# Performance work log

Hardware: AMD Instinct MI355X
Metric: run time of the kernel (lower is better)

Reference implementation:

```python
import jax, jax.numpy as jnp
import numpy as np

B, N = 65536, 128

def setup_inputs() -> dict:
    key = jax.random.key(0)
    k1, k2, k3, k4, k5 = jax.random.split(key, 5)
    density = jax.random.uniform(k1, (B, N), dtype=jnp.float32) * 10.0   # nonneg densities
    deltas = jax.random.uniform(k2, (B, N), dtype=jnp.float32) * 0.05 + 1e-3  # positive step sizes
    zs = jnp.cumsum(deltas, axis=-1) + 2.0                               # monotone sample depths
    raw_rgbs = jax.random.uniform(k4, (B, N, 3), dtype=jnp.float32)
    raw_normals = jax.random.normal(k5, (B, N, 3), dtype=jnp.float32)
    return {"density": density, "deltas": deltas, "zs": zs,
            "raw_rgbs": raw_rgbs, "raw_normals": raw_normals}


def reference(density, deltas, zs, raw_rgbs, raw_normals):
    # alpha -> transmittance (exclusive cumprod) -> weight
    alpha = 1.0 - jnp.exp(-density * deltas)                 # [B, N]
    one_minus = 1.0 - alpha
    cp = jnp.cumprod(one_minus, axis=-1)                     # inclusive cumprod
    trans = jnp.concatenate([jnp.ones_like(cp[:, :1]), cp[:, :-1]], axis=-1)  # exclusive
    weight = alpha * trans                                   # [B, N]

    # composites
    rgb = jnp.einsum('bn,bnc->bc', weight, raw_rgbs)         # [B, 3]
    acc = jnp.sum(weight, axis=1, keepdims=True)             # [B, 1]
    depth = jnp.sum(weight * zs, axis=1, keepdims=True) / (acc + 1e-8)  # normalized
    normal = jnp.einsum('bn,bnc->bc', weight, raw_normals)   # [B, 3]

    # pack outputs: rgb(3) | depth(1) | normal(3) | acc(1) -> [B, 8]
    return jnp.concatenate([rgb, depth, normal, acc], axis=-1)
```

## Files before the change

### kernel.cpp

```cpp
#include <hip/hip_runtime.h>


constexpr int RAYS = 65536;
constexpr int NS   = 128;

__global__ __launch_bounds__(256) void render_composite_kernel(
    const float* __restrict__ density,
    const float* __restrict__ deltas,
    const float* __restrict__ zs,
    const float* __restrict__ rgbs,
    const float* __restrict__ normals,
    float* __restrict__ out)
{
    const int lane = threadIdx.x & 63;
    const int wave = threadIdx.x >> 6;
    const int ray  = blockIdx.x * 4 + wave;
    if (ray >= RAYS) return;

    const size_t row  = (size_t)ray * NS;
    const size_t row3 = (size_t)ray * NS * 3;

    const float2 d  = reinterpret_cast<const float2*>(density + row)[lane];
    const float2 dl = reinterpret_cast<const float2*>(deltas  + row)[lane];
    const float2 z  = reinterpret_cast<const float2*>(zs      + row)[lane];

    const float s0 = d.x * dl.x;
    const float s1 = d.y * dl.y;
    const float slocal = s0 + s1;

    float prefix = slocal;
    #pragma unroll
    for (int off = 1; off < 64; off <<= 1) {
        float up = __shfl_up(prefix, off, 64);
        if (lane >= off) prefix += up;
    }
    const float S_base = prefix - slocal;

    const float e0 = __expf(-S_base);
    const float e1 = __expf(-(S_base + s0));
    const float e2 = __expf(-(S_base + s0 + s1));
    const float w0 = e0 - e1;
    const float w1 = e1 - e2;

    const float2* rg2 = reinterpret_cast<const float2*>(rgbs    + row3) + lane * 3;
    const float2* nm2 = reinterpret_cast<const float2*>(normals + row3) + lane * 3;
    const float2 ra = rg2[0], rb = rg2[1], rc = rg2[2];
    const float2 na = nm2[0], nb = nm2[1], nc = nm2[2];

    float acc_r = w0 * ra.x + w1 * rb.y;
    float acc_g = w0 * ra.y + w1 * rc.x;
    float acc_b = w0 * rb.x + w1 * rc.y;
    float acc_nr = w0 * na.x + w1 * nb.y;
    float acc_ng = w0 * na.y + w1 * nc.x;
    float acc_nb = w0 * nb.x + w1 * nc.y;
    float acc_w  = w0 + w1;
    float acc_wz = w0 * z.x + w1 * z.y;

    #pragma unroll
    for (int off = 32; off > 0; off >>= 1) {
        acc_r  += __shfl_xor(acc_r,  off, 64);
        acc_g  += __shfl_xor(acc_g,  off, 64);
        acc_b  += __shfl_xor(acc_b,  off, 64);
        acc_nr += __shfl_xor(acc_nr, off, 64);
        acc_ng += __shfl_xor(acc_ng, off, 64);
        acc_nb += __shfl_xor(acc_nb, off, 64);
        acc_w  += __shfl_xor(acc_w,  off, 64);
        acc_wz += __shfl_xor(acc_wz, off, 64);
    }

    if (lane == 0) {
        const float depth = acc_wz / (acc_w + 1e-8f);
        float4* o = reinterpret_cast<float4*>(out + (size_t)ray * 8);
        o[0] = make_float4(acc_r, acc_g, acc_b, depth);
        o[1] = make_float4(acc_nr, acc_ng, acc_nb, acc_w);
    }
}

extern "C" void kernel_launch(void* const* d_in, const int* in_sizes, int n_in,
                              void* d_out, int out_size, void* d_ws, size_t ws_size,
                              hipStream_t stream) {
    const float* density = (const float*)d_in[0];
    const float* deltas  = (const float*)d_in[1];
    const float* zs      = (const float*)d_in[2];
    const float* rgbs    = (const float*)d_in[3];
    const float* normals = (const float*)d_in[4];
    float* out = (float*)d_out;

    const int waves_per_block = 4;
    const int grid = RAYS / waves_per_block;
    render_composite_kernel<<<grid, 256, 0, stream>>>(
        density, deltas, zs, rgbs, normals, out);
}
```

Measured before the change: 278.5 us.

## Map two rays per wave with float4 loads and DPP-based half-wave scans

Each 64-lane wave now handles two rays, one per 32-lane half, and each lane processes four samples through float4 loads instead of two through float2. The prefix scan and the eight reductions switch from ds_bpermute-style shuffles to DPP row operations (row_shr plus row_bcast15) over 32 lanes, and the final lane of each half writes the result. This is meant to cut shuffle latency and instruction count and to widen memory transactions. The trade-off is more registers per lane and a hand-written DPP scan whose correctness depends on the exact control encodings.

```diff
diff --git a/kernel.cpp b/kernel.cpp
--- a/kernel.cpp
+++ b/kernel.cpp
@@ -3,6 +3,19 @@
 
 constexpr int RAYS = 65536;
 constexpr int NS   = 128;
+
+#define DPP_ADD(x, ctrl, rm)                                                   \
+    x += __int_as_float(__builtin_amdgcn_update_dpp(                           \
+        0, __float_as_int(x), ctrl, rm, 0xf, true))
+
+__device__ __forceinline__ float scan32(float x) {
+    DPP_ADD(x, 0x111, 0xf);
+    DPP_ADD(x, 0x112, 0xf);
+    DPP_ADD(x, 0x114, 0xf);
+    DPP_ADD(x, 0x118, 0xf);
+    DPP_ADD(x, 0x142, 0xa);
+    return x;
+}
 
 __global__ __launch_bounds__(256) void render_composite_kernel(
     const float* __restrict__ density,
@@ -12,63 +25,65 @@
     const float* __restrict__ normals,
     float* __restrict__ out)
 {
-    const int lane = threadIdx.x & 63;
-    const int wave = threadIdx.x >> 6;
-    const int ray  = blockIdx.x * 4 + wave;
-    if (ray >= RAYS) return;
+    const int tid  = threadIdx.x;
+    const int lane = tid & 63;
+    const int k    = lane & 31;
+    const int ray  = blockIdx.x * 8 + (tid >> 6) * 2 + (lane >> 5);
 
     const size_t row  = (size_t)ray * NS;
     const size_t row3 = (size_t)ray * NS * 3;
 
-    const float2 d  = reinterpret_cast<const float2*>(density + row)[lane];
-    const float2 dl = reinterpret_cast<const float2*>(deltas  + row)[lane];
-    const float2 z  = reinterpret_cast<const float2*>(zs      + row)[lane];
+    const float4 d  = reinterpret_cast<const float4*>(density + row)[k];
+    const float4 dl = reinterpret_cast<const float4*>(deltas  + row)[k];
+    const float4 z  = reinterpret_cast<const float4*>(zs      + row)[k];
+
+    const float4* rg = reinterpret_cast<const float4*>(rgbs    + row3) + k * 3;
+    const float4* nm = reinterpret_cast<const float4*>(normals + row3) + k * 3;
+    const float4 r0 = rg[0], r1 = rg[1], r2 = rg[2];
+    const float4 n0 = nm[0], n1 = nm[1], n2 = nm[2];
 
     const float s0 = d.x * dl.x;
     const float s1 = d.y * dl.y;
-    const float slocal = s0 + s1;
+    const float s2 = d.z * dl.z;
+    const float s3 = d.w * dl.w;
+    const float slocal = (s0 + s1) + (s2 + s3);
 
-    float prefix = slocal;
-    #pragma unroll
-    for (int off = 1; off < 64; off <<= 1) {
-        float up = __shfl_up(prefix, off, 64);
-        if (lane >= off) prefix += up;
-    }
-    const float S_base = prefix - slocal;
+    const float prefix = scan32(slocal);
+    const float S0 = prefix - slocal;
+    const float S1 = S0 + s0;
+    const float S2 = S1 + s1;
+    const float S3 = S2 + s2;
+    const float S4 = S3 + s3;
 
-    const float e0 = __expf(-S_base);
-    const float e1 = __expf(-(S_base + s0));
-    const float e2 = __expf(-(S_base + s0 + s1));
+    const float e0 = __expf(-S0);
+    const float e1 = __expf(-S1);
+    const float e2 = __expf(-S2);
+    const float e3 = __expf(-S3);
+    const float e4 = __expf(-S4);
     const float w0 = e0 - e1;
     const float w1 = e1 - e2;
+    const float w2 = e2 - e3;
+    const float w3 = e3 - e4;
 
-    const float2* rg2 = reinterpret_cast<const float2*>(rgbs    + row3) + lane * 3;
-    const float2* nm2 = reinterpret_cast<const float2*>(normals + row3) + lane * 3;
-    const float2 ra = rg2[0], rb = rg2[1], rc = rg2[2];
-    const float2 na = nm2[0], nb = nm2[1], nc = nm2[2];
+    float acc_r  = w0 * r0.x + w1 * r0.w + w2 * r1.z + w3 * r2.y;
+    float acc_g  = w0 * r0.y + w1 * r1.x + w2 * r1.w + w3 * r2.z;
+    float acc_b  = w0 * r0.z + w1 * r1.y + w2 * r2.x + w3 * r2.w;
+    float acc_nr = w0 * n0.x + w1 * n0.w + w2 * n1.z + w3 * n2.y;
+    float acc_ng = w0 * n0.y + w1 * n1.x + w2 * n1.w + w3 * n2.z;
+    float acc_nb = w0 * n0.z + w1 * n1.y + w2 * n2.x + w3 * n2.w;
+    float acc_w  = (w0 + w1) + (w2 + w3);
+    float acc_wz = w0 * z.x + w1 * z.y + w2 * z.z + w3 * z.w;
 
-    float acc_r = w0 * ra.x + w1 * rb.y;
-    float acc_g = w0 * ra.y + w1 * rc.x;
-    float acc_b = w0 * rb.x + w1 * rc.y;
-    float acc_nr = w0 * na.x + w1 * nb.y;
-    float acc_ng = w0 * na.y + w1 * nc.x;
-    float acc_nb = w0 * nb.x + w1 * nc.y;
-    float acc_w  = w0 + w1;
-    float acc_wz = w0 * z.x + w1 * z.y;
+    acc_r  = scan32(acc_r);
+    acc_g  = scan32(acc_g);
+    acc_b  = scan32(acc_b);
+    acc_nr = scan32(acc_nr);
+    acc_ng = scan32(acc_ng);
+    acc_nb = scan32(acc_nb);
+    acc_w  = scan32(acc_w);
+    acc_wz = scan32(acc_wz);
 
-    #pragma unroll
-    for (int off = 32; off > 0; off >>= 1) {
-        acc_r  += __shfl_xor(acc_r,  off, 64);
-        acc_g  += __shfl_xor(acc_g,  off, 64);
-        acc_b  += __shfl_xor(acc_b,  off, 64);
-        acc_nr += __shfl_xor(acc_nr, off, 64);
-        acc_ng += __shfl_xor(acc_ng, off, 64);
-        acc_nb += __shfl_xor(acc_nb, off, 64);
-        acc_w  += __shfl_xor(acc_w,  off, 64);
-        acc_wz += __shfl_xor(acc_wz, off, 64);
-    }
-
-    if (lane == 0) {
+    if (k == 31) {
         const float depth = acc_wz / (acc_w + 1e-8f);
         float4* o = reinterpret_cast<float4*>(out + (size_t)ray * 8);
         o[0] = make_float4(acc_r, acc_g, acc_b, depth);
@@ -86,8 +101,7 @@
     const float* normals = (const float*)d_in[4];
     float* out = (float*)d_out;
 
-    const int waves_per_block = 4;
-    const int grid = RAYS / waves_per_block;
+    const int grid = RAYS / 8;
     render_composite_kernel<<<grid, 256, 0, stream>>>(
         density, deltas, zs, rgbs, normals, out);
 }
```

Measured after the change: 278.9 us. About the same (+0.1%).
